# Performance work log

Measured on AMD Instinct MI355X. Metric: run time of the kernel, lower is better.

## Reference

```python
import jax, jax.numpy as jnp
import numpy as np

B, C, H, W = 16, 512, 64, 64
G = 32
CG = C // G       # per-group channels = 16


def setup_inputs() -> dict:
    key = jax.random.key(0)
    ks = jax.random.split(key, 6)
    def w(k, shape, fan_in):
        return (jax.random.normal(k, shape, jnp.float32) / np.float32(np.sqrt(fan_in)))
    return {
        "x": jax.random.normal(ks[0], (B, C, H, W), jnp.float32),
        "conv1_w": w(ks[1], (CG, CG), CG), "conv1_b": jnp.zeros((CG,), jnp.float32),
        "convh_w": w(ks[2], (CG, CG), CG), "convh_b": jnp.zeros((CG,), jnp.float32),
        "convw_w": w(ks[3], (CG, CG), CG), "convw_b": jnp.zeros((CG,), jnp.float32),
        "conv3_w": w(ks[4], (CG, CG, 3, 3), CG * 9), "conv3_b": jnp.zeros((CG,), jnp.float32),
        "gn_w": jnp.ones((CG,), jnp.float32), "gn_b": jnp.zeros((CG,), jnp.float32),
    }


def _conv1x1(y, w, b):
    # y: [N, Ci, L]  w: [Co, Ci]  -> [N, Co, L]
    return jnp.einsum('oi,bil->bol', w, y) + b[None, :, None]


def _ema_forward(x, conv1_w, conv1_b, convh_w, convh_b, convw_w, convw_b,
                 conv3_w, conv3_b, gn_w, gn_b):
    b, c, h, w = x.shape
    g, cg, hw = G, CG, h * w
    bg = b * g
    xg = x.reshape(bg, cg, h, w)

    # coordinate pooling: row means [bg,cg,h], col means [bg,cg,w]
    x_h = xg.mean(axis=3)                     # [bg, cg, h]
    x_w = xg.mean(axis=2)                     # [bg, cg, w]
    y = jnp.concatenate([x_h, x_w], axis=2)   # [bg, cg, h+w]
    y = jax.nn.relu(_conv1x1(y, conv1_w, conv1_b))
    y_h, y_w = y[:, :, :h], y[:, :, h:]

    a_h = jax.nn.sigmoid(_conv1x1(y_h, convh_w, convh_b))[:, :, :, None]  # [bg,cg,h,1]
    a_w = jax.nn.sigmoid(_conv1x1(y_w, convw_w, convw_b))[:, :, None, :]  # [bg,cg,1,w]

    x1 = xg * a_h * a_w

    # GroupNorm(num_groups=1): normalize over (cg,h,w) per sample, affine per channel
    mu = x1.mean(axis=(1, 2, 3), keepdims=True)
    var = ((x1 - mu) ** 2).mean(axis=(1, 2, 3), keepdims=True)
    x2 = (x1 - mu) * jax.lax.rsqrt(var + 1e-5)
    x2 = x2 * gn_w[None, :, None, None] + gn_b[None, :, None, None]

    # 3x3 conv branch
    x3 = jax.lax.conv_general_dilated(
        xg, conv3_w, window_strides=(1, 1), padding='SAME',
        dimension_numbers=('NCHW', 'OIHW', 'NCHW'))
    x3 = jax.nn.relu(x3 + conv3_b[None, :, None, None])

    A2 = jax.nn.softmax(x2.reshape(bg, cg, hw), axis=-1)  # [bg,cg,hw]
    A3 = jax.nn.softmax(x3.reshape(bg, cg, hw), axis=-1)
    V2 = x2.mean(axis=(2, 3))                              # [bg,cg]
    V3 = x3.mean(axis=(2, 3))

    s2 = jnp.einsum('bc,bcl->bl', V2, A3)  # [bg, hw]
    s3 = jnp.einsum('bc,bcl->bl', V3, A2)
    s = jax.nn.softmax(s2 + s3, axis=-1).reshape(bg, 1, h, w)

    return (xg * s).reshape(b, c, h, w)


def reference(x, conv1_w, conv1_b, convh_w, convh_b, convw_w, convw_b,
              conv3_w, conv3_b, gn_w, gn_b):
    return _ema_forward(x, conv1_w, conv1_b, convh_w, convh_b, convw_w, convw_b,
                        conv3_w, conv3_b, gn_w, gn_b)
```

## Files before the change

### kernel.cpp

```cpp
#include <hip/hip_runtime.h>
#include <hip/hip_bf16.h>

#define CHW4 16384
#define STR  84

__device__ __forceinline__ float wred(float v){
#pragma unroll
  for (int o = 32; o; o >>= 1) v += __shfl_xor(v, o, 64);
  return v;
}
__device__ __forceinline__ float wred16(float v){
#pragma unroll
  for (int o = 8; o; o >>= 1) v += __shfl_xor(v, o, 64);
  return v;
}
__device__ __forceinline__ float bf2f(unsigned short u){
  return __uint_as_float(((unsigned)u) << 16);
}
__device__ __forceinline__ unsigned short f2b(float f){
  union { __hip_bfloat16 h; unsigned short u; } cv;
  cv.h = __float2bfloat16(f);
  return cv.u;
}

__global__ __launch_bounds__(1024, 4) void ema_fused(const float* __restrict__ x,
    const float* __restrict__ w1, const float* __restrict__ b1,
    const float* __restrict__ wh, const float* __restrict__ bh,
    const float* __restrict__ ww, const float* __restrict__ bw,
    const float* __restrict__ w3, const float* __restrict__ b3,
    const float* __restrict__ gnw, const float* __restrict__ gnb,
    float* __restrict__ out)
{
  __shared__ __align__(16) unsigned short E3s[16*4096];
  __shared__ __align__(16) float uni[6720];
  __shared__ float v3p[128], z3p[128];
  __shared__ float chpart[256], zpart[256];
  __shared__ float red1[16], red2[16];
  __shared__ float murs[2];
  __shared__ float sc_s[16], of_s[16], v2_s[16], p2s[16], p3s[16];
  __shared__ float invS_s;

  const int tid = threadIdx.x;
  const int bg  = blockIdx.x;
  const float4* x4 = (const float4*)x + (size_t)bg * CHW4;
  float4* o4 = (float4*)out + (size_t)bg * CHW4;

  const int lane = tid & 63;
  const int unit = __builtin_amdgcn_readfirstlane(tid >> 8);
  const int ut   = tid & 255;
  const int cog  = __builtin_amdgcn_readfirstlane((tid & 255) >> 6);
  const int co0  = cog * 4;
  const int cr   = lane >> 3;
  const int w0   = (lane & 7) * 8;
  float* in_u = &uni[unit * 1680];

  const int q0  = ut % 18, rr0 = (ut / 18) % 10, c20 = ut / 180;
  const int ut1 = ut + 256;
  const int q1  = ut1 % 18, rr1 = (ut1 / 18) % 10, c21 = ut1 / 180;
  const bool have1 = (ut < 104);

  float acc[4][8];
#pragma unroll
  for (int i = 0; i < 4; ++i)
#pragma unroll
    for (int px = 0; px < 8; ++px) acc[i][px] = 0.f;

  float4 pa, pb;
  {
    int hb = unit*16 - 1;
    pa = make_float4(0.f,0.f,0.f,0.f); pb = make_float4(0.f,0.f,0.f,0.f);
    int hh0 = hb + rr0;
    if (q0 >= 1 && q0 <= 16 && (unsigned)hh0 < 64u)
      pa = x4[c20*1024 + hh0*16 + (q0-1)];
    if (have1){
      int hh1 = hb + rr1;
      if (q1 >= 1 && q1 <= 16 && (unsigned)hh1 < 64u)
        pb = x4[c21*1024 + hh1*16 + (q1-1)];
    }
  }

#pragma unroll 1
  for (int round = 0; round < 16; ++round){
    __syncthreads();
    *(float4*)&in_u[(c20*10 + rr0)*STR + q0*4] = pa;
    if (have1) *(float4*)&in_u[(c21*10 + rr1)*STR + q1*4] = pb;
    __syncthreads();
    if (round < 15){
      int rn = round + 1;
      int sg = unit*2 + (rn >> 3);
      int cb = (rn & 7) * 2;
      int hb = sg*8 - 1;
      pa = make_float4(0.f,0.f,0.f,0.f); pb = make_float4(0.f,0.f,0.f,0.f);
      int hh0 = hb + rr0;
      if (q0 >= 1 && q0 <= 16 && (unsigned)hh0 < 64u)
        pa = x4[(cb + c20)*1024 + hh0*16 + (q0-1)];
      if (have1){
        int hh1 = hb + rr1;
        if (q1 >= 1 && q1 <= 16 && (unsigned)hh1 < 64u)
          pb = x4[(cb + c21)*1024 + hh1*16 + (q1-1)];
      }
    }
    const int ch2 = (round & 7) * 2;
#pragma unroll
    for (int c2 = 0; c2 < 2; ++c2){
      const int ci = ch2 + c2;
      float wgt[4][9];
#pragma unroll
      for (int i = 0; i < 4; ++i)
#pragma unroll
        for (int t = 0; t < 9; ++t)
          wgt[i][t] = w3[((co0+i)*16 + ci)*9 + t];
#pragma unroll
      for (int dy = 0; dy < 3; ++dy){
        const float* rowp = &in_u[(c2*10 + cr + dy)*STR + w0];
        float4 A0  = *(const float4*)(rowp);
        float4 A1  = *(const float4*)(rowp+4);
        float4 A2v = *(const float4*)(rowp+8);
        float4 A3v = *(const float4*)(rowp+12);
        float v[16] = {A0.x,A0.y,A0.z,A0.w, A1.x,A1.y,A1.z,A1.w,
                       A2v.x,A2v.y,A2v.z,A2v.w, A3v.x,A3v.y,A3v.z,A3v.w};
#pragma unroll
        for (int dx = 0; dx < 3; ++dx)
#pragma unroll
          for (int px = 0; px < 8; ++px){
            float iv = v[px + dx + 3];
#pragma unroll
            for (int i = 0; i < 4; ++i)
              acc[i][px] = fmaf(wgt[i][dy*3+dx], iv, acc[i][px]);
          }
      }
    }
    if ((round & 7) == 7){
      const int sg = unit*2 + (round >> 3);
      const int hh = sg*8 + cr;
#pragma unroll
      for (int i = 0; i < 4; ++i){
        float bias = b3[co0+i];
        union { unsigned short hb16[8]; uint4 u; } pk;
        float v3acc = 0.f, z3acc = 0.f;
#pragma unroll
        for (int px = 0; px < 8; ++px){
          float val = fmaxf(acc[i][px] + bias, 0.f);
          float e = __expf(val);
          v3acc += val; z3acc += e;
          pk.hb16[px] = f2b(e);
          acc[i][px] = 0.f;
        }
        *(uint4*)&E3s[(co0+i)*4096 + hh*64 + w0] = pk.u;
        float rv = wred(v3acc);
        float rz = wred(z3acc);
        if (lane == 0){
          v3p[sg*16 + co0 + i] = rv;
          z3p[sg*16 + co0 + i] = rz;
        }
      }
    }
  }

  float* rs  = uni;
  float* cs  = uni + 1024;
  float* ym  = uni + 2048;
  float* ahs = uni + 4096;
  float* aws = uni + 5120;
  const int h   = tid >> 4;
  const int w4i = tid & 15;
  const int wv  = tid >> 6;

  __syncthreads();
  cs[tid] = 0.f;
  __syncthreads();
#pragma unroll 8
  for (int k = 0; k < 16; ++k){
    float4 v = x4[k*1024 + tid];
    float srow = v.x + v.y + v.z + v.w;
    srow = wred16(srow);
    if ((tid & 15) == 0) rs[k*64 + h] = srow;
    v.x += __shfl_xor(v.x, 16); v.x += __shfl_xor(v.x, 32);
    v.y += __shfl_xor(v.y, 16); v.y += __shfl_xor(v.y, 32);
    v.z += __shfl_xor(v.z, 16); v.z += __shfl_xor(v.z, 32);
    v.w += __shfl_xor(v.w, 16); v.w += __shfl_xor(v.w, 32);
    if (lane < 16){
      atomicAdd(&cs[k*64 + lane*4 + 0], v.x);
      atomicAdd(&cs[k*64 + lane*4 + 1], v.y);
      atomicAdd(&cs[k*64 + lane*4 + 2], v.z);
      atomicAdd(&cs[k*64 + lane*4 + 3], v.w);
    }
  }
  __syncthreads();
  for (int ol = tid; ol < 2048; ol += 1024){
    int o = ol >> 7, l = ol & 127;
    float a = b1[o];
#pragma unroll
    for (int i = 0; i < 16; ++i){
      float mv = (l < 64 ? rs[i*64 + l] : cs[i*64 + (l-64)]) * (1.f/64.f);
      a = fmaf(w1[o*16 + i], mv, a);
    }
    ym[o*128 + l] = fmaxf(a, 0.f);
  }
  __syncthreads();
  for (int ol = tid; ol < 2048; ol += 1024){
    int q = ol >> 10;
    int o = (ol >> 6) & 15;
    int p = ol & 63;
    const float* Wm = q ? ww : wh;
    float a = q ? bw[o] : bh[o];
#pragma unroll
    for (int i = 0; i < 16; ++i)
      a = fmaf(Wm[o*16 + i], ym[i*128 + q*64 + p], a);
    float sgm = 1.f / (1.f + __expf(-a));
    (q ? aws : ahs)[o*64 + p] = sgm;
  }
  __syncthreads();

  const float4* aws4 = (const float4*)aws;
  float s1 = 0.f, s2 = 0.f;
#pragma unroll 8
  for (int k = 0; k < 16; ++k){
    float4 v = x4[k*1024 + tid];
    float ah = ahs[k*64 + h];
    float4 aw = aws4[k*16 + w4i];
    float4 x1;
    x1.x = v.x * ah * aw.x;
    x1.y = v.y * ah * aw.y;
    x1.z = v.z * ah * aw.z;
    x1.w = v.w * ah * aw.w;
    float csum = x1.x + x1.y + x1.z + x1.w;
    s1 += csum;
    s2 = fmaf(x1.x, x1.x, s2); s2 = fmaf(x1.y, x1.y, s2);
    s2 = fmaf(x1.z, x1.z, s2); s2 = fmaf(x1.w, x1.w, s2);
    float cw = wred(csum);
    if (lane == 0) chpart[k*16 + wv] = cw;
  }
  float r1 = wred(s1), r2 = wred(s2);
  if (lane == 0){ red1[wv] = r1; red2[wv] = r2; }
  __syncthreads();
  if (tid == 0){
    float S = 0.f, SS = 0.f;
#pragma unroll
    for (int i = 0; i < 16; ++i){ S += red1[i]; SS += red2[i]; }
    float mu  = S * (1.f/65536.f);
    float var = SS * (1.f/65536.f) - mu*mu;
    murs[0] = mu; murs[1] = rsqrtf(var + 1e-5f);
  }
  __syncthreads();
  if (tid < 16){
    float ch = 0.f;
#pragma unroll
    for (int m = 0; m < 16; ++m) ch += chpart[tid*16 + m];
    float mu = murs[0], rstd = murs[1];
    float g = gnw[tid], b = gnb[tid];
    float sc = rstd * g;
    sc_s[tid] = sc; of_s[tid] = b - mu*sc;
    v2_s[tid] = (ch * (1.f/4096.f) - mu) * sc + b;
  }
  __syncthreads();

  unsigned e2a[16], e2b[16];
#pragma unroll
  for (int k = 0; k < 16; ++k){
    float4 v = x4[k*1024 + tid];
    float ah = ahs[k*64 + h];
    float4 aw = aws4[k*16 + w4i];
    float sc = sc_s[k], of = of_s[k];
    float ex = __expf(fmaf(v.x * ah * aw.x, sc, of));
    float ey = __expf(fmaf(v.y * ah * aw.y, sc, of));
    float ez = __expf(fmaf(v.z * ah * aw.z, sc, of));
    float ew = __expf(fmaf(v.w * ah * aw.w, sc, of));
    float z = ex + ey + ez + ew;
    e2a[k] = (unsigned)f2b(ex) | ((unsigned)f2b(ey) << 16);
    e2b[k] = (unsigned)f2b(ez) | ((unsigned)f2b(ew) << 16);
    float zw = wred(z);
    if (lane == 0) zpart[k*16 + wv] = zw;
  }
  __syncthreads();
  if (tid < 16){
    float z2 = 0.f;
#pragma unroll
    for (int m = 0; m < 16; ++m) z2 += zpart[tid*16 + m];
    float v3 = 0.f, z3 = 0.f;
#pragma unroll
    for (int ss = 0; ss < 8; ++ss){
      v3 += v3p[ss*16 + tid];
      z3 += z3p[ss*16 + tid];
    }
    p2s[tid] = v3 * (1.f/4096.f) / z2;
    p3s[tid] = v2_s[tid] / z3;
  }
  __syncthreads();

  float4 tacc = make_float4(0.f,0.f,0.f,0.f);
#pragma unroll
  for (int k = 0; k < 16; ++k){
    ushort4 eu = *(const ushort4*)&E3s[k*4096 + tid*4];
    float p2 = p2s[k], p3 = p3s[k];
    tacc.x += bf2f((unsigned short)(e2a[k] & 0xffffu))*p2 + bf2f(eu.x)*p3;
    tacc.y += bf2f((unsigned short)(e2a[k] >> 16))   *p2 + bf2f(eu.y)*p3;
    tacc.z += bf2f((unsigned short)(e2b[k] & 0xffffu))*p2 + bf2f(eu.z)*p3;
    tacc.w += bf2f((unsigned short)(e2b[k] >> 16))   *p2 + bf2f(eu.w)*p3;
  }
  float4 e;
  e.x = __expf(tacc.x); e.y = __expf(tacc.y);
  e.z = __expf(tacc.z); e.w = __expf(tacc.w);
  float es = e.x + e.y + e.z + e.w;
  float rr = wred(es);
  if (lane == 0) red1[wv] = rr;
  __syncthreads();
  if (tid == 0){
    float S = 0.f;
#pragma unroll
    for (int i = 0; i < 16; ++i) S += red1[i];
    invS_s = 1.f / S;
  }
  __syncthreads();
  float iS = invS_s;
  float4 ei = make_float4(e.x*iS, e.y*iS, e.z*iS, e.w*iS);

#pragma unroll 8
  for (int k = 0; k < 16; ++k){
    float4 v = x4[k*1024 + tid];
    float4 ov;
    ov.x = v.x * ei.x; ov.y = v.y * ei.y;
    ov.z = v.z * ei.z; ov.w = v.w * ei.w;
    o4[k*1024 + tid] = ov;
  }
}

extern "C" void kernel_launch(void* const* d_in, const int* in_sizes, int n_in,
                              void* d_out, int out_size, void* d_ws, size_t ws_size,
                              hipStream_t stream)
{
  const float* x   = (const float*)d_in[0];
  const float* w1  = (const float*)d_in[1];
  const float* b1  = (const float*)d_in[2];
  const float* wh  = (const float*)d_in[3];
  const float* bh  = (const float*)d_in[4];
  const float* ww  = (const float*)d_in[5];
  const float* bw  = (const float*)d_in[6];
  const float* w3  = (const float*)d_in[7];
  const float* b3  = (const float*)d_in[8];
  const float* gnw = (const float*)d_in[9];
  const float* gnb = (const float*)d_in[10];
  float* out = (float*)d_out;
  (void)d_ws; (void)ws_size; (void)n_in; (void)in_sizes; (void)out_size;

  ema_fused<<<dim3(512), 1024, 0, stream>>>(x, w1, b1, wh, bh, ww, bw,
                                            w3, b3, gnw, gnb, out);
}
```

Before: 542.8 us.

## Fuse row/column pooling into conv tile loop and interleave LDS halo layout

The separate pass that re-read all of x from global memory to compute row and column sums is removed. Those sums are now computed inside the 3x3 conv rounds from the tile already staged in LDS, using shuffles and LDS atomics. The LDS tile is also reorganized into an even/odd float4 interleaved layout with a narrower stride, to reduce bank conflicts on the conv reads and to free shared memory. The cost is extra reduction work and atomics in every conv round, plus more complex index math.

```diff
diff --git a/kernel.cpp b/kernel.cpp
--- a/kernel.cpp
+++ b/kernel.cpp
@@ -2,7 +2,7 @@
 #include <hip/hip_bf16.h>
 
 #define CHW4 16384
-#define STR  84
+#define STRD 72
 
 __device__ __forceinline__ float wred(float v){
 #pragma unroll
@@ -31,14 +31,10 @@
     const float* __restrict__ gnw, const float* __restrict__ gnb,
     float* __restrict__ out)
 {
-  __shared__ __align__(16) unsigned short E3s[16*4096];
-  __shared__ __align__(16) float uni[6720];
+  __shared__ __align__(16) unsigned short E3s[65536];
+  __shared__ float rs_s[1024], cs_s[1024];
   __shared__ float v3p[128], z3p[128];
-  __shared__ float chpart[256], zpart[256];
-  __shared__ float red1[16], red2[16];
-  __shared__ float murs[2];
-  __shared__ float sc_s[16], of_s[16], v2_s[16], p2s[16], p3s[16];
-  __shared__ float invS_s;
+  __shared__ __align__(16) float scr[5760];
 
   const int tid = threadIdx.x;
   const int bg  = blockIdx.x;
@@ -51,13 +47,23 @@
   const int cog  = __builtin_amdgcn_readfirstlane((tid & 255) >> 6);
   const int co0  = cog * 4;
   const int cr   = lane >> 3;
-  const int w0   = (lane & 7) * 8;
-  float* in_u = &uni[unit * 1680];
-
-  const int q0  = ut % 18, rr0 = (ut / 18) % 10, c20 = ut / 180;
+  const int cc   = lane & 7;
+  float* in_u = scr + unit * 1440;
+
+  const int p0 = ut % 18, rr0 = (ut / 18) % 10, c20 = ut / 180;
+  const int sl0 = (p0 <= 8) ? 2*p0 : 2*(p0-9)+1;
   const int ut1 = ut + 256;
-  const int q1  = ut1 % 18, rr1 = (ut1 / 18) % 10, c21 = ut1 / 180;
+  const int p1 = ut1 % 18, rr1 = (ut1 / 18) % 10, c21 = ut1 / 180;
+  const int sl1 = (p1 <= 8) ? 2*p1 : 2*(p1-9)+1;
   const bool have1 = (ut < 104);
+
+  const int pc2  = ut >> 7;
+  const int prow = (ut >> 4) & 7;
+  const int wseg = ut & 15;
+  const int sPP  = wseg + 1;
+  const int pPP  = (sPP >> 1) + 9*(sPP & 1);
+
+  cs_s[tid] = 0.f;
 
   float acc[4][8];
 #pragma unroll
@@ -70,40 +76,41 @@
     int hb = unit*16 - 1;
     pa = make_float4(0.f,0.f,0.f,0.f); pb = make_float4(0.f,0.f,0.f,0.f);
     int hh0 = hb + rr0;
-    if (q0 >= 1 && q0 <= 16 && (unsigned)hh0 < 64u)
-      pa = x4[c20*1024 + hh0*16 + (q0-1)];
+    if (sl0 >= 1 && sl0 <= 16 && (unsigned)hh0 < 64u)
+      pa = x4[c20*1024 + hh0*16 + (sl0-1)];
     if (have1){
       int hh1 = hb + rr1;
-      if (q1 >= 1 && q1 <= 16 && (unsigned)hh1 < 64u)
-        pb = x4[c21*1024 + hh1*16 + (q1-1)];
+      if (sl1 >= 1 && sl1 <= 16 && (unsigned)hh1 < 64u)
+        pb = x4[c21*1024 + hh1*16 + (sl1-1)];
     }
   }
 
 #pragma unroll 1
   for (int round = 0; round < 16; ++round){
     __syncthreads();
-    *(float4*)&in_u[(c20*10 + rr0)*STR + q0*4] = pa;
-    if (have1) *(float4*)&in_u[(c21*10 + rr1)*STR + q1*4] = pb;
+    *(float4*)&in_u[(c20*10 + rr0)*STRD + p0*4] = pa;
+    if (have1) *(float4*)&in_u[(c21*10 + rr1)*STRD + p1*4] = pb;
     __syncthreads();
     if (round < 15){
       int rn = round + 1;
-      int sg = unit*2 + (rn >> 3);
-      int cb = (rn & 7) * 2;
-      int hb = sg*8 - 1;
+      int sgn = unit*2 + (rn >> 3);
+      int cbn = (rn & 7) * 2;
+      int hb = sgn*8 - 1;
       pa = make_float4(0.f,0.f,0.f,0.f); pb = make_float4(0.f,0.f,0.f,0.f);
       int hh0 = hb + rr0;
-      if (q0 >= 1 && q0 <= 16 && (unsigned)hh0 < 64u)
-        pa = x4[(cb + c20)*1024 + hh0*16 + (q0-1)];
+      if (sl0 >= 1 && sl0 <= 16 && (unsigned)hh0 < 64u)
+        pa = x4[(cbn + c20)*1024 + hh0*16 + (sl0-1)];
       if (have1){
         int hh1 = hb + rr1;
-        if (q1 >= 1 && q1 <= 16 && (unsigned)hh1 < 64u)
-          pb = x4[(cb + c21)*1024 + hh1*16 + (q1-1)];
+        if (sl1 >= 1 && sl1 <= 16 && (unsigned)hh1 < 64u)
+          pb = x4[(cbn + c21)*1024 + hh1*16 + (sl1-1)];
       }
     }
-    const int ch2 = (round & 7) * 2;
+    const int cb = (round & 7) * 2;
+    const int sg = unit*2 + (round >> 3);
 #pragma unroll
     for (int c2 = 0; c2 < 2; ++c2){
-      const int ci = ch2 + c2;
+      const int ci = cb + c2;
       float wgt[4][9];
 #pragma unroll
       for (int i = 0; i < 4; ++i)
@@ -112,11 +119,11 @@
           wgt[i][t] = w3[((co0+i)*16 + ci)*9 + t];
 #pragma unroll
       for (int dy = 0; dy < 3; ++dy){
-        const float* rowp = &in_u[(c2*10 + cr + dy)*STR + w0];
-        float4 A0  = *(const float4*)(rowp);
-        float4 A1  = *(const float4*)(rowp+4);
-        float4 A2v = *(const float4*)(rowp+8);
-        float4 A3v = *(const float4*)(rowp+12);
+        const float* rowp = &in_u[(c2*10 + cr + dy)*STRD];
+        float4 A0  = *(const float4*)(rowp + 4*cc);
+        float4 A1  = *(const float4*)(rowp + 4*(cc+9));
+        float4 A2v = *(const float4*)(rowp + 4*(cc+1));
+        float4 A3v = *(const float4*)(rowp + 4*(cc+10));
         float v[16] = {A0.x,A0.y,A0.z,A0.w, A1.x,A1.y,A1.z,A1.w,
                        A2v.x,A2v.y,A2v.z,A2v.w, A3v.x,A3v.y,A3v.z,A3v.w};
 #pragma unroll
@@ -130,8 +137,24 @@
           }
       }
     }
+    {
+      float4 pv = *(const float4*)&in_u[(pc2*10 + 1 + prow)*STRD + pPP*4];
+      int ci = cb + pc2;
+      float rsum = pv.x + pv.y + pv.z + pv.w;
+      rsum = wred16(rsum);
+      if ((lane & 15) == 0) rs_s[ci*64 + sg*8 + prow] = rsum;
+      pv.x += __shfl_xor(pv.x,16); pv.x += __shfl_xor(pv.x,32);
+      pv.y += __shfl_xor(pv.y,16); pv.y += __shfl_xor(pv.y,32);
+      pv.z += __shfl_xor(pv.z,16); pv.z += __shfl_xor(pv.z,32);
+      pv.w += __shfl_xor(pv.w,16); pv.w += __shfl_xor(pv.w,32);
+      if (lane < 16){
+        atomicAdd(&cs_s[ci*64 + wseg*4 + 0], pv.x);
+        atomicAdd(&cs_s[ci*64 + wseg*4 + 1], pv.y);
+        atomicAdd(&cs_s[ci*64 + wseg*4 + 2], pv.z);
+        atomicAdd(&cs_s[ci*64 + wseg*4 + 3], pv.w);
+      }
+    }
     if ((round & 7) == 7){
-      const int sg = unit*2 + (round >> 3);
       const int hh = sg*8 + cr;
 #pragma unroll
       for (int i = 0; i < 4; ++i){
@@ -146,7 +169,7 @@
           pk.hb16[px] = f2b(e);
           acc[i][px] = 0.f;
         }
-        *(uint4*)&E3s[(co0+i)*4096 + hh*64 + w0] = pk.u;
+        *(uint4*)&E3s[(co0+i)*4096 + hh*64 + cc*8] = pk.u;
         float rv = wred(v3acc);
         float rz = wred(z3acc);
         if (lane == 0){
@@ -157,42 +180,33 @@
     }
   }
 
-  float* rs  = uni;
-  float* cs  = uni + 1024;
-  float* ym  = uni + 2048;
-  float* ahs = uni + 4096;
-  float* aws = uni + 5120;
+  float* ym  = scr;
+  float* ahs = scr + 2048;
+  float* aws = scr + 3072;
+  float* chpart = scr + 4096;
+  float* zpart  = scr + 4352;
+  float* red1   = scr + 4608;
+  float* red2   = scr + 4624;
+  float* murs   = scr + 4640;
+  float* sc_s   = scr + 4656;
+  float* of_s   = scr + 4672;
+  float* v2_s   = scr + 4688;
+  float* p2s    = scr + 4704;
+  float* p3s    = scr + 4720;
+  float* invS   = scr + 4736;
+
   const int h   = tid >> 4;
   const int w4i = tid & 15;
   const int wv  = tid >> 6;
 
   __syncthreads();
-  cs[tid] = 0.f;
-  __syncthreads();
-#pragma unroll 8
-  for (int k = 0; k < 16; ++k){
-    float4 v = x4[k*1024 + tid];
-    float srow = v.x + v.y + v.z + v.w;
-    srow = wred16(srow);
-    if ((tid & 15) == 0) rs[k*64 + h] = srow;
-    v.x += __shfl_xor(v.x, 16); v.x += __shfl_xor(v.x, 32);
-    v.y += __shfl_xor(v.y, 16); v.y += __shfl_xor(v.y, 32);
-    v.z += __shfl_xor(v.z, 16); v.z += __shfl_xor(v.z, 32);
-    v.w += __shfl_xor(v.w, 16); v.w += __shfl_xor(v.w, 32);
-    if (lane < 16){
-      atomicAdd(&cs[k*64 + lane*4 + 0], v.x);
-      atomicAdd(&cs[k*64 + lane*4 + 1], v.y);
-      atomicAdd(&cs[k*64 + lane*4 + 2], v.z);
-      atomicAdd(&cs[k*64 + lane*4 + 3], v.w);
-    }
-  }
-  __syncthreads();
+
   for (int ol = tid; ol < 2048; ol += 1024){
     int o = ol >> 7, l = ol & 127;
     float a = b1[o];
 #pragma unroll
     for (int i = 0; i < 16; ++i){
-      float mv = (l < 64 ? rs[i*64 + l] : cs[i*64 + (l-64)]) * (1.f/64.f);
+      float mv = (l < 64 ? rs_s[i*64 + l] : cs_s[i*64 + (l-64)]) * (1.f/64.f);
       a = fmaf(w1[o*16 + i], mv, a);
     }
     ym[o*128 + l] = fmaxf(a, 0.f);
@@ -309,10 +323,10 @@
     float S = 0.f;
 #pragma unroll
     for (int i = 0; i < 16; ++i) S += red1[i];
-    invS_s = 1.f / S;
-  }
-  __syncthreads();
-  float iS = invS_s;
+    invS[0] = 1.f / S;
+  }
+  __syncthreads();
+  float iS = invS[0];
   float4 ei = make_float4(e.x*iS, e.y*iS, e.z*iS, e.w*iS);
 
 #pragma unroll 8
```

After: 689.4 us. +27.0%, slower.
